# Kernel tuning notes

Measured on AMD Instinct MI355X. Metric: run time of the kernel, lower is better.

Reference implementation:

```python
import jax, jax.numpy as jnp
import numpy as np

B, T, I, H, C = 4096, 64, 60, 60, 600


def setup_inputs() -> dict:
    key = jax.random.key(0)
    ks = jax.random.split(key, 7)
    s = 1.0 / np.sqrt(H).astype(np.float32)  # PyTorch RNN init bound
    u = lambda k, shape: jax.random.uniform(k, shape, jnp.float32, -s, s)
    return {
        "x": jax.random.normal(ks[0], (B, T, I), jnp.float32),
        "w_ih": u(ks[1], (2, 3 * H, I)),   # per-direction [3H, I], gates (r,z,n)
        "w_hh": u(ks[2], (2, 3 * H, H)),
        "b_ih": u(ks[3], (2, 3 * H)),
        "b_hh": u(ks[4], (2, 3 * H)),
        "fc_w": u(ks[5], (C, 2 * H * T)),
        "fc_b": u(ks[6], (C,)),
    }


def _gru_dir(x_tbi, w_ih, w_hh, b_ih, b_hh):
    # Precompute input-side gate pre-activations for all timesteps: [T, B, 3H]
    gx = jnp.einsum('tbi,gi->tbg', x_tbi, w_ih) + b_ih
    h0 = jnp.zeros((x_tbi.shape[1], H), x_tbi.dtype)

    def step(h, gx_t):
        gh = h @ w_hh.T + b_hh                      # [B, 3H]
        r = jax.nn.sigmoid(gx_t[:, :H] + gh[:, :H])
        z = jax.nn.sigmoid(gx_t[:, H:2 * H] + gh[:, H:2 * H])
        n = jnp.tanh(gx_t[:, 2 * H:] + r * gh[:, 2 * H:])
        h_new = (1.0 - z) * n + z * h
        return h_new, h_new

    _, hs = jax.lax.scan(step, h0, gx)
    return hs  # [T, B, H]


def reference(x, w_ih, w_hh, b_ih, b_hh, fc_w, fc_b):
    xt = jnp.swapaxes(x, 0, 1)                        # [T, B, I]
    fwd = _gru_dir(xt, w_ih[0], w_hh[0], b_ih[0], b_hh[0])           # [T,B,H]
    bwd = _gru_dir(xt[::-1], w_ih[1], w_hh[1], b_ih[1], b_hh[1])[::-1]
    out = jnp.concatenate([fwd, bwd], axis=-1)        # [T, B, 2H]
    out = jnp.swapaxes(out, 0, 1).reshape(x.shape[0], -1)  # [B, T*2H]
    return out @ fc_w.T + fc_b
```

## Files before the change

kernel.cpp:

```cpp
#include <hip/hip_runtime.h>

#define BB 4096
#define TT 64
#define NH 60
#define KF 7680
#define NC 600

typedef short bf16x8 __attribute__((ext_vector_type(8)));
typedef float f32x4 __attribute__((ext_vector_type(4)));
#define MFMA16(A,B,C) __builtin_amdgcn_mfma_f32_16x16x32_bf16(A,B,C,0,0,0)

__device__ __forceinline__ unsigned short f2bf(float v) {
    unsigned int u = __float_as_uint(v);
    return (unsigned short)((u + 0x7FFFu + ((u >> 16) & 1u)) >> 16);
}
__device__ __forceinline__ float bf2f(unsigned short b) {
    return __uint_as_float(((unsigned int)b) << 16);
}
__device__ __forceinline__ float sigf(float v)     { return 1.f / (1.f + __expf(-v)); }
__device__ __forceinline__ float tanhfast(float v) { return 2.f / (1.f + __expf(-2.f * v)) - 1.f; }

__global__ __launch_bounds__(512, 2) void gru4_kernel(
    const float* __restrict__ x,
    const float* __restrict__ w_ih,
    const float* __restrict__ w_hh,
    const float* __restrict__ b_ih,
    const float* __restrict__ b_hh,
    unsigned int* __restrict__ hs)
{
    __shared__ unsigned short XHh[2][32 * 128];
    __shared__ unsigned short XHl[2][32 * 128];
    __shared__ unsigned int hstage[2][32][60];

    const int tid = threadIdx.x;
    const int d  = blockIdx.y;
    const int b0 = blockIdx.x * 32;
    const int wave = tid >> 6, lane = tid & 63;
    const int mtile = wave >> 2, ug = wave & 3;
    const int l15 = lane & 15, lq = lane >> 4;
    const int j = ug * 16 + l15;
    const bool jv = j < NH;
    const int m = mtile * 16 + l15;
    const int rbase = mtile * 16 + lq * 4;

    for (int i = tid; i < 2 * 32 * 128; i += 512) { (&XHh[0][0])[i] = 0; (&XHl[0][0])[i] = 0; }

    bf16x8 wHf[3][4], wLf[3][4];
#pragma unroll
    for (int g = 0; g < 3; ++g) {
#pragma unroll
        for (int kt = 0; kt < 4; ++kt) {
            bf16x8 h8, l8;
            const int kb = kt * 32 + lq * 8;
#pragma unroll
            for (int e = 0; e < 8; ++e) {
                const int k = kb + e;
                float v = 0.f;
                if (jv) {
                    if (k < 60)                    v = w_ih[(size_t)d * 10800 + (g * 60 + j) * 60 + k];
                    else if (k >= 64 && k < 124)   v = w_hh[(size_t)d * 10800 + (g * 60 + j) * 60 + (k - 64)];
                }
                const unsigned short hb = f2bf(v);
                const unsigned short lb = f2bf(v - bf2f(hb));
                h8[e] = (short)hb; l8[e] = (short)lb;
            }
            wHf[g][kt] = h8; wLf[g][kt] = l8;
        }
    }

    float bir = 0, biz = 0, bin = 0, bhr = 0, bhz = 0, bhn = 0;
    if (jv) {
        bir = b_ih[d * 180 + j]; biz = b_ih[d * 180 + 60 + j]; bin = b_ih[d * 180 + 120 + j];
        bhr = b_hh[d * 180 + j]; bhz = b_hh[d * 180 + 60 + j]; bhn = b_hh[d * 180 + 120 + j];
    }

    const bool xact = tid < 480;
    const int rowx = xact ? tid / 15 : 31;
    const int cx   = xact ? tid % 15 : 14;
    const float* xb = x + ((size_t)(b0 + rowx) * TT) * 60 + cx * 4;
    unsigned int* hsb = hs + (size_t)(b0 + rowx) * KF + d * 60 + cx * 4;

    __syncthreads();

    if (xact) {
        const int tt0 = d ? (TT - 1) : 0;
        const float4 v = *(const float4*)(xb + tt0 * 60);
        const float vv[4] = {v.x, v.y, v.z, v.w};
#pragma unroll
        for (int e = 0; e < 4; ++e) {
            const int k = cx * 4 + e;
            const int idx = rowx * 128 + (((k >> 3) ^ (rowx & 7)) << 3) + (k & 7);
            const unsigned short hb = f2bf(vv[e]);
            XHh[0][idx] = hb; XHl[0][idx] = f2bf(vv[e] - bf2f(hb));
        }
    }
    float hold[4] = {0.f, 0.f, 0.f, 0.f};
    __syncthreads();

#pragma unroll 2
    for (int s = 0; s < TT; ++s) {
        const int p = s & 1, pn = p ^ 1;
        const int tt = d ? (TT - 1 - s) : s;

        float4 xp = make_float4(0.f, 0.f, 0.f, 0.f);
        const bool morex = (s < TT - 1) && xact;
        if (morex) xp = *(const float4*)(xb + (d ? (TT - 2 - s) : (s + 1)) * 60);

        f32x4 aR0 = {0,0,0,0}, aR1 = {0,0,0,0}, aZ0 = {0,0,0,0}, aZ1 = {0,0,0,0},
              aNX = {0,0,0,0}, aNH_ = {0,0,0,0};
        const unsigned short* Xh = &XHh[p][0];
        const unsigned short* Xl = &XHl[p][0];
#pragma unroll
        for (int kt = 0; kt < 4; ++kt) {
            const int c = kt * 4 + lq;
            const int off = m * 128 + ((c ^ (m & 7)) << 3);
            const bf16x8 aH = *(const bf16x8*)(Xh + off);
            const bf16x8 aL = *(const bf16x8*)(Xl + off);
            if (kt < 2) {
                aR0 = MFMA16(aH, wHf[0][kt], aR0); aR0 = MFMA16(aH, wLf[0][kt], aR0); aR0 = MFMA16(aL, wHf[0][kt], aR0);
                aZ0 = MFMA16(aH, wHf[1][kt], aZ0); aZ0 = MFMA16(aH, wLf[1][kt], aZ0); aZ0 = MFMA16(aL, wHf[1][kt], aZ0);
                aNX = MFMA16(aH, wHf[2][kt], aNX); aNX = MFMA16(aH, wLf[2][kt], aNX); aNX = MFMA16(aL, wHf[2][kt], aNX);
            } else {
                aR1 = MFMA16(aH, wHf[0][kt], aR1); aR1 = MFMA16(aH, wLf[0][kt], aR1); aR1 = MFMA16(aL, wHf[0][kt], aR1);
                aZ1 = MFMA16(aH, wHf[1][kt], aZ1); aZ1 = MFMA16(aH, wLf[1][kt], aZ1); aZ1 = MFMA16(aL, wHf[1][kt], aZ1);
                aNH_ = MFMA16(aH, wHf[2][kt], aNH_); aNH_ = MFMA16(aH, wLf[2][kt], aNH_); aNH_ = MFMA16(aL, wHf[2][kt], aNH_);
            }
        }

        float hnew[4];
#pragma unroll
        for (int r = 0; r < 4; ++r) {
            const float rr = sigf(aR0[r] + aR1[r] + bir + bhr);
            const float zz = sigf(aZ0[r] + aZ1[r] + biz + bhz);
            const float nn = tanhfast(aNX[r] + bin + rr * (aNH_[r] + bhn));
            hnew[r] = (1.f - zz) * nn + zz * hold[r];
            hold[r] = hnew[r];
        }

        if (jv) {
#pragma unroll
            for (int r = 0; r < 4; ++r) {
                const int rw = rbase + r;
                const int k = 64 + j;
                const int idx = rw * 128 + (((k >> 3) ^ (rw & 7)) << 3) + (k & 7);
                const unsigned short hb = f2bf(hnew[r]);
                const unsigned short lb = f2bf(hnew[r] - bf2f(hb));
                XHh[pn][idx] = hb; XHl[pn][idx] = lb;
                hstage[pn][rw][j] = ((unsigned int)hb << 16) | lb;
            }
        }
        if (morex) {
            const float vv[4] = {xp.x, xp.y, xp.z, xp.w};
#pragma unroll
            for (int e = 0; e < 4; ++e) {
                const int k = cx * 4 + e;
                const int idx = rowx * 128 + (((k >> 3) ^ (rowx & 7)) << 3) + (k & 7);
                const unsigned short hb = f2bf(vv[e]);
                XHh[pn][idx] = hb; XHl[pn][idx] = f2bf(vv[e] - bf2f(hb));
            }
        }
        __syncthreads();

        if (xact) {
            const uint4 hv = *(const uint4*)&hstage[pn][rowx][cx * 4];
            *(uint4*)(hsb + (size_t)tt * 120) = hv;
        }
    }
}

__global__ void out_init_kernel(const float* __restrict__ fcb, float* __restrict__ out) {
    const int i = blockIdx.x * 1024 + threadIdx.x;
    out[i] = fcb[i % NC];
}

__global__ __launch_bounds__(512, 2) void fc4_kernel(
    const unsigned int* __restrict__ hs,
    const float* __restrict__ fcw,
    float* __restrict__ out)
{
    __shared__ unsigned short Ash[2][256 * 64];
    __shared__ unsigned short Bsh[2][128 * 64];

    const int tid = threadIdx.x;
    const int m0 = blockIdx.x * 256;
    const int n0 = blockIdx.y * 128;
    const int k0 = blockIdx.z * 2560;
    const int wave = tid >> 6, lane = tid & 63;
    const int wm = wave >> 1, wn = wave & 1;
    const int l15 = lane & 15, lq = lane >> 4;

    f32x4 acc[4][4];
#pragma unroll
    for (int a = 0; a < 4; ++a)
#pragma unroll
        for (int b = 0; b < 4; ++b) acc[a][b] = (f32x4){0, 0, 0, 0};

    uint4 pa[4]; float4 pb[2];

#define STAGE_LOAD(t) do {                                                          \
    const int kc_ = k0 + (t) * 32;                                                  \
    _Pragma("unroll")                                                               \
    for (int it = 0; it < 4; ++it) {                                                \
        const int g_ = tid + it * 512, row_ = g_ >> 3, qi_ = g_ & 7;                \
        pa[it] = *(const uint4*)(hs + (size_t)(m0 + row_) * KF + kc_ + qi_ * 4);    \
    }                                                                               \
    _Pragma("unroll")                                                               \
    for (int it = 0; it < 2; ++it) {                                                \
        const int g_ = tid + it * 512, row_ = g_ >> 3, qi_ = g_ & 7;                \
        const int cc_ = n0 + row_;                                                  \
        pb[it] = (cc_ < NC) ? *(const float4*)(fcw + (size_t)cc_ * KF + kc_ + qi_ * 4) \
                            : make_float4(0.f, 0.f, 0.f, 0.f);                      \
    }                                                                               \
} while (0)

#define STAGE_WRITE(buf) do {                                                       \
    _Pragma("unroll")                                                               \
    for (int it = 0; it < 4; ++it) {                                                \
        const int g_ = tid + it * 512, row_ = g_ >> 3, qi_ = g_ & 7;                \
        const int ch_ = qi_ >> 1, hf_ = qi_ & 1;                                    \
        unsigned short* base_ = &Ash[buf][row_ * 64];                               \
        uint2 wh_, wl_;                                                             \
        wh_.x = (pa[it].x >> 16) | (pa[it].y & 0xFFFF0000u);                        \
        wh_.y = (pa[it].z >> 16) | (pa[it].w & 0xFFFF0000u);                        \
        wl_.x = (pa[it].x & 0xFFFFu) | (pa[it].y << 16);                            \
        wl_.y = (pa[it].z & 0xFFFFu) | (pa[it].w << 16);                            \
        *(uint2*)(base_ + ((ch_ ^ (row_ & 7)) << 3) + hf_ * 4) = wh_;               \
        *(uint2*)(base_ + (((ch_ | 4) ^ (row_ & 7)) << 3) + hf_ * 4) = wl_;         \
    }                                                                               \
    _Pragma("unroll")                                                               \
    for (int it = 0; it < 2; ++it) {                                                \
        const int g_ = tid + it * 512, row_ = g_ >> 3, qi_ = g_ & 7;                \
        const int ch_ = qi_ >> 1, hf_ = qi_ & 1;                                    \
        unsigned short* base_ = &Bsh[buf][row_ * 64];                               \
        const float bv_[4] = {pb[it].x, pb[it].y, pb[it].z, pb[it].w};              \
        unsigned short h4_[4], l4_[4];                                              \
        _Pragma("unroll")                                                           \
        for (int e = 0; e < 4; ++e) { h4_[e] = f2bf(bv_[e]); l4_[e] = f2bf(bv_[e] - bf2f(h4_[e])); } \
        uint2 wh_, wl_;                                                             \
        wh_.x = (unsigned int)h4_[0] | ((unsigned int)h4_[1] << 16);                \
        wh_.y = (unsigned int)h4_[2] | ((unsigned int)h4_[3] << 16);                \
        wl_.x = (unsigned int)l4_[0] | ((unsigned int)l4_[1] << 16);                \
        wl_.y = (unsigned int)l4_[2] | ((unsigned int)l4_[3] << 16);                \
        *(uint2*)(base_ + ((ch_ ^ (row_ & 7)) << 3) + hf_ * 4) = wh_;               \
        *(uint2*)(base_ + (((ch_ | 4) ^ (row_ & 7)) << 3) + hf_ * 4) = wl_;         \
    }                                                                               \
} while (0)

#define MFMA_PHASE(buf) do {                                                        \
    const unsigned short* Ab_ = &Ash[buf][0];                                       \
    const unsigned short* Bb_ = &Bsh[buf][0];                                       \
    bf16x8 aH_[4], aL_[4], bH_[4], bL_[4];                                          \
    _Pragma("unroll")                                                               \
    for (int t = 0; t < 4; ++t) {                                                   \
        const int mr_ = wm * 64 + t * 16 + l15;                                     \
        const unsigned short* p_ = Ab_ + mr_ * 64;                                  \
        aH_[t] = *(const bf16x8*)(p_ + ((lq ^ (mr_ & 7)) << 3));                    \
        aL_[t] = *(const bf16x8*)(p_ + (((lq | 4) ^ (mr_ & 7)) << 3));              \
        const int nr_ = wn * 64 + t * 16 + l15;                                     \
        const unsigned short* q_ = Bb_ + nr_ * 64;                                  \
        bH_[t] = *(const bf16x8*)(q_ + ((lq ^ (nr_ & 7)) << 3));                    \
        bL_[t] = *(const bf16x8*)(q_ + (((lq | 4) ^ (nr_ & 7)) << 3));              \
    }                                                                               \
    _Pragma("unroll")                                                               \
    for (int mt = 0; mt < 4; ++mt)                                                  \
        _Pragma("unroll")                                                           \
        for (int nt = 0; nt < 4; ++nt) {                                            \
            acc[mt][nt] = MFMA16(aH_[mt], bH_[nt], acc[mt][nt]);                    \
            acc[mt][nt] = MFMA16(aH_[mt], bL_[nt], acc[mt][nt]);                    \
            acc[mt][nt] = MFMA16(aL_[mt], bH_[nt], acc[mt][nt]);                    \
        }                                                                           \
} while (0)

#define BARRIER_LGKM() do {                                                         \
    asm volatile("s_waitcnt lgkmcnt(0)" ::: "memory");                              \
    __builtin_amdgcn_s_barrier();                                                   \
    __builtin_amdgcn_sched_barrier(0);                                              \
} while (0)

    STAGE_LOAD(0);
    STAGE_WRITE(0);
    STAGE_LOAD(1);
    __syncthreads();

#pragma unroll 1
    for (int t = 0; t < 80; t += 2) {
        STAGE_WRITE(1);
        if (t + 2 < 80) STAGE_LOAD(t + 2);
        MFMA_PHASE(0);
        BARRIER_LGKM();
        if (t + 2 < 80) STAGE_WRITE(0);
        if (t + 3 < 80) STAGE_LOAD(t + 3);
        MFMA_PHASE(1);
        BARRIER_LGKM();
    }

#pragma unroll
    for (int mt = 0; mt < 4; ++mt) {
        const int row = m0 + wm * 64 + mt * 16 + lq * 4;
#pragma unroll
        for (int nt = 0; nt < 4; ++nt) {
            const int col = n0 + wn * 64 + nt * 16 + l15;
            if (col < NC) {
#pragma unroll
                for (int r = 0; r < 4; ++r)
                    atomicAdd(out + (size_t)(row + r) * NC + col, acc[mt][nt][r]);
            }
        }
    }
#undef STAGE_LOAD
#undef STAGE_WRITE
#undef MFMA_PHASE
#undef BARRIER_LGKM
}

extern "C" void kernel_launch(void* const* d_in, const int* in_sizes, int n_in,
                              void* d_out, int out_size, void* d_ws, size_t ws_size,
                              hipStream_t stream) {
    (void)in_sizes; (void)n_in; (void)out_size;
    const float* x    = (const float*)d_in[0];
    const float* w_ih = (const float*)d_in[1];
    const float* w_hh = (const float*)d_in[2];
    const float* b_ih = (const float*)d_in[3];
    const float* b_hh = (const float*)d_in[4];
    const float* fcw  = (const float*)d_in[5];
    const float* fcb  = (const float*)d_in[6];
    float* out = (float*)d_out;
    unsigned int* hs = (unsigned int*)d_ws;

    if (ws_size < (size_t)KF * BB * sizeof(unsigned int)) return;

    out_init_kernel<<<dim3((BB * NC) / 1024), 1024, 0, stream>>>(fcb, out);
    gru4_kernel<<<dim3(BB / 32, 2), 512, 0, stream>>>(x, w_ih, w_hh, b_ih, b_hh, hs);
    fc4_kernel<<<dim3(BB / 256, 5, 3), 512, 0, stream>>>(hs, fcw, out);
}
```

Baseline: 365.6 us.

## Shrink GRU blocks, use direct global-to-LDS loads and drop FC weight low part

```diff
diff --git a/kernel.cpp b/kernel.cpp
--- a/kernel.cpp
+++ b/kernel.cpp
@@ -10,6 +10,9 @@
 typedef float f32x4 __attribute__((ext_vector_type(4)));
 #define MFMA16(A,B,C) __builtin_amdgcn_mfma_f32_16x16x32_bf16(A,B,C,0,0,0)
 
+typedef const __attribute__((address_space(1))) unsigned int* gas_u32;
+typedef __attribute__((address_space(3))) unsigned int* las_u32;
+
 __device__ __forceinline__ unsigned short f2bf(float v) {
     unsigned int u = __float_as_uint(v);
     return (unsigned short)((u + 0x7FFFu + ((u >> 16) & 1u)) >> 16);
@@ -20,7 +23,21 @@
 __device__ __forceinline__ float sigf(float v)     { return 1.f / (1.f + __expf(-v)); }
 __device__ __forceinline__ float tanhfast(float v) { return 2.f / (1.f + __expf(-2.f * v)) - 1.f; }
 
-__global__ __launch_bounds__(512, 2) void gru4_kernel(
+__device__ __forceinline__ void unpk(const uint4 a, const uint4 b, bf16x8& hi, bf16x8& lo) {
+    uint4 h, l;
+    h.x = (a.x >> 16) | (a.y & 0xFFFF0000u);
+    h.y = (a.z >> 16) | (a.w & 0xFFFF0000u);
+    h.z = (b.x >> 16) | (b.y & 0xFFFF0000u);
+    h.w = (b.z >> 16) | (b.w & 0xFFFF0000u);
+    l.x = (a.x & 0xFFFFu) | (a.y << 16);
+    l.y = (a.z & 0xFFFFu) | (a.w << 16);
+    l.z = (b.x & 0xFFFFu) | (b.y << 16);
+    l.w = (b.z & 0xFFFFu) | (b.w << 16);
+    hi = __builtin_bit_cast(bf16x8, h);
+    lo = __builtin_bit_cast(bf16x8, l);
+}
+
+__global__ __launch_bounds__(256, 2) void gru5_kernel(
     const float* __restrict__ x,
     const float* __restrict__ w_ih,
     const float* __restrict__ w_hh,
@@ -28,22 +45,22 @@
     const float* __restrict__ b_hh,
     unsigned int* __restrict__ hs)
 {
-    __shared__ unsigned short XHh[2][32 * 128];
-    __shared__ unsigned short XHl[2][32 * 128];
-    __shared__ unsigned int hstage[2][32][60];
+    __shared__ unsigned short XHh[2][16 * 128];
+    __shared__ unsigned short XHl[2][16 * 128];
+    __shared__ unsigned int hstage[2][16][60];
 
     const int tid = threadIdx.x;
     const int d  = blockIdx.y;
-    const int b0 = blockIdx.x * 32;
+    const int b0 = blockIdx.x * 16;
     const int wave = tid >> 6, lane = tid & 63;
-    const int mtile = wave >> 2, ug = wave & 3;
+    const int ug = wave;
     const int l15 = lane & 15, lq = lane >> 4;
     const int j = ug * 16 + l15;
     const bool jv = j < NH;
-    const int m = mtile * 16 + l15;
-    const int rbase = mtile * 16 + lq * 4;
-
-    for (int i = tid; i < 2 * 32 * 128; i += 512) { (&XHh[0][0])[i] = 0; (&XHl[0][0])[i] = 0; }
+    const int m = l15;
+    const int rbase = lq * 4;
+
+    for (int i = tid; i < 2 * 16 * 128; i += 256) { (&XHh[0][0])[i] = 0; (&XHl[0][0])[i] = 0; }
 
     bf16x8 wHf[3][4], wLf[3][4];
 #pragma unroll
@@ -74,8 +91,8 @@
         bhr = b_hh[d * 180 + j]; bhz = b_hh[d * 180 + 60 + j]; bhn = b_hh[d * 180 + 120 + j];
     }
 
-    const bool xact = tid < 480;
-    const int rowx = xact ? tid / 15 : 31;
+    const bool xact = tid < 240;
+    const int rowx = xact ? tid / 15 : 15;
     const int cx   = xact ? tid % 15 : 14;
     const float* xb = x + ((size_t)(b0 + rowx) * TT) * 60 + cx * 4;
     unsigned int* hsb = hs + (size_t)(b0 + rowx) * KF + d * 60 + cx * 4;
@@ -97,7 +114,7 @@
     float hold[4] = {0.f, 0.f, 0.f, 0.f};
     __syncthreads();
 
-#pragma unroll 2
+#pragma unroll 1
     for (int s = 0; s < TT; ++s) {
         const int p = s & 1, pn = p ^ 1;
         const int tt = d ? (TT - 1 - s) : s;
@@ -173,18 +190,18 @@
     out[i] = fcb[i % NC];
 }
 
-__global__ __launch_bounds__(512, 2) void fc4_kernel(
+__global__ __launch_bounds__(512, 1) void fc5_kernel(
     const unsigned int* __restrict__ hs,
     const float* __restrict__ fcw,
     float* __restrict__ out)
 {
-    __shared__ unsigned short Ash[2][256 * 64];
-    __shared__ unsigned short Bsh[2][128 * 64];
+    __shared__ unsigned int  Apk[2][256 * 32];
+    __shared__ unsigned short Bs[2][128 * 32];
 
     const int tid = threadIdx.x;
     const int m0 = blockIdx.x * 256;
     const int n0 = blockIdx.y * 128;
-    const int k0 = blockIdx.z * 2560;
+    const int k0 = blockIdx.z * 1280;
     const int wave = tid >> 6, lane = tid & 63;
     const int wm = wave >> 1, wn = wave & 1;
     const int l15 = lane & 15, lq = lane >> 4;
@@ -195,103 +212,94 @@
 #pragma unroll
         for (int b = 0; b < 4; ++b) acc[a][b] = (f32x4){0, 0, 0, 0};
 
-    uint4 pa[4]; float4 pb[2];
-
-#define STAGE_LOAD(t) do {                                                          \
-    const int kc_ = k0 + (t) * 32;                                                  \
-    _Pragma("unroll")                                                               \
-    for (int it = 0; it < 4; ++it) {                                                \
-        const int g_ = tid + it * 512, row_ = g_ >> 3, qi_ = g_ & 7;                \
-        pa[it] = *(const uint4*)(hs + (size_t)(m0 + row_) * KF + kc_ + qi_ * 4);    \
-    }                                                                               \
-    _Pragma("unroll")                                                               \
-    for (int it = 0; it < 2; ++it) {                                                \
-        const int g_ = tid + it * 512, row_ = g_ >> 3, qi_ = g_ & 7;                \
-        const int cc_ = n0 + row_;                                                  \
-        pb[it] = (cc_ < NC) ? *(const float4*)(fcw + (size_t)cc_ * KF + kc_ + qi_ * 4) \
-                            : make_float4(0.f, 0.f, 0.f, 0.f);                      \
-    }                                                                               \
+    const int ga_row = lane >> 3;
+    const int ga_chk = (lane & 7) ^ ga_row;
+
+#define STAGE_A(buf, kc_) do {                                                        \
+    _Pragma("unroll")                                                                 \
+    for (int c_ = 0; c_ < 4; ++c_) {                                                  \
+        const int bc_ = wave * 4 + c_;                                                \
+        const unsigned int* g_ = hs + (size_t)(m0 + bc_ * 8 + ga_row) * KF            \
+                                    + (kc_) + (ga_chk << 2);                          \
+        __builtin_amdgcn_global_load_lds((gas_u32)g_, (las_u32)&Apk[buf][bc_ * 256],  \
+                                         16, 0, 0);                                   \
+    }                                                                                 \
 } while (0)
 
-#define STAGE_WRITE(buf) do {                                                       \
-    _Pragma("unroll")                                                               \
-    for (int it = 0; it < 4; ++it) {                                                \
-        const int g_ = tid + it * 512, row_ = g_ >> 3, qi_ = g_ & 7;                \
-        const int ch_ = qi_ >> 1, hf_ = qi_ & 1;                                    \
-        unsigned short* base_ = &Ash[buf][row_ * 64];                               \
-        uint2 wh_, wl_;                                                             \
-        wh_.x = (pa[it].x >> 16) | (pa[it].y & 0xFFFF0000u);                        \
-        wh_.y = (pa[it].z >> 16) | (pa[it].w & 0xFFFF0000u);                        \
-        wl_.x = (pa[it].x & 0xFFFFu) | (pa[it].y << 16);                            \
-        wl_.y = (pa[it].z & 0xFFFFu) | (pa[it].w << 16);                            \
-        *(uint2*)(base_ + ((ch_ ^ (row_ & 7)) << 3) + hf_ * 4) = wh_;               \
-        *(uint2*)(base_ + (((ch_ | 4) ^ (row_ & 7)) << 3) + hf_ * 4) = wl_;         \
-    }                                                                               \
-    _Pragma("unroll")                                                               \
-    for (int it = 0; it < 2; ++it) {                                                \
-        const int g_ = tid + it * 512, row_ = g_ >> 3, qi_ = g_ & 7;                \
-        const int ch_ = qi_ >> 1, hf_ = qi_ & 1;                                    \
-        unsigned short* base_ = &Bsh[buf][row_ * 64];                               \
-        const float bv_[4] = {pb[it].x, pb[it].y, pb[it].z, pb[it].w};              \
-        unsigned short h4_[4], l4_[4];                                              \
-        _Pragma("unroll")                                                           \
-        for (int e = 0; e < 4; ++e) { h4_[e] = f2bf(bv_[e]); l4_[e] = f2bf(bv_[e] - bf2f(h4_[e])); } \
-        uint2 wh_, wl_;                                                             \
-        wh_.x = (unsigned int)h4_[0] | ((unsigned int)h4_[1] << 16);                \
-        wh_.y = (unsigned int)h4_[2] | ((unsigned int)h4_[3] << 16);                \
-        wl_.x = (unsigned int)l4_[0] | ((unsigned int)l4_[1] << 16);                \
-        wl_.y = (unsigned int)l4_[2] | ((unsigned int)l4_[3] << 16);                \
-        *(uint2*)(base_ + ((ch_ ^ (row_ & 7)) << 3) + hf_ * 4) = wh_;               \
-        *(uint2*)(base_ + (((ch_ | 4) ^ (row_ & 7)) << 3) + hf_ * 4) = wl_;         \
-    }                                                                               \
+    float4 pb[2];
+#define LOAD_B(kc_) do {                                                              \
+    _Pragma("unroll")                                                                 \
+    for (int it = 0; it < 2; ++it) {                                                  \
+        const int g_ = tid + it * 512, row_ = g_ >> 3, qi_ = g_ & 7;                  \
+        const int cc_ = n0 + row_;                                                    \
+        pb[it] = (cc_ < NC) ? *(const float4*)(fcw + (size_t)cc_ * KF + (kc_) + qi_ * 4) \
+                            : make_float4(0.f, 0.f, 0.f, 0.f);                        \
+    }                                                                                 \
 } while (0)
 
-#define MFMA_PHASE(buf) do {                                                        \
-    const unsigned short* Ab_ = &Ash[buf][0];                                       \
-    const unsigned short* Bb_ = &Bsh[buf][0];                                       \
-    bf16x8 aH_[4], aL_[4], bH_[4], bL_[4];                                          \
-    _Pragma("unroll")                                                               \
-    for (int t = 0; t < 4; ++t) {                                                   \
-        const int mr_ = wm * 64 + t * 16 + l15;                                     \
-        const unsigned short* p_ = Ab_ + mr_ * 64;                                  \
-        aH_[t] = *(const bf16x8*)(p_ + ((lq ^ (mr_ & 7)) << 3));                    \
-        aL_[t] = *(const bf16x8*)(p_ + (((lq | 4) ^ (mr_ & 7)) << 3));              \
-        const int nr_ = wn * 64 + t * 16 + l15;                                     \
-        const unsigned short* q_ = Bb_ + nr_ * 64;                                  \
-        bH_[t] = *(const bf16x8*)(q_ + ((lq ^ (nr_ & 7)) << 3));                    \
-        bL_[t] = *(const bf16x8*)(q_ + (((lq | 4) ^ (nr_ & 7)) << 3));              \
-    }                                                                               \
-    _Pragma("unroll")                                                               \
-    for (int mt = 0; mt < 4; ++mt)                                                  \
-        _Pragma("unroll")                                                           \
-        for (int nt = 0; nt < 4; ++nt) {                                            \
-            acc[mt][nt] = MFMA16(aH_[mt], bH_[nt], acc[mt][nt]);                    \
-            acc[mt][nt] = MFMA16(aH_[mt], bL_[nt], acc[mt][nt]);                    \
-            acc[mt][nt] = MFMA16(aL_[mt], bH_[nt], acc[mt][nt]);                    \
-        }                                                                           \
+#define WRITE_B(buf) do {                                                             \
+    _Pragma("unroll")                                                                 \
+    for (int it = 0; it < 2; ++it) {                                                  \
+        const int g_ = tid + it * 512, row_ = g_ >> 3, qi_ = g_ & 7;                  \
+        const int ch_ = qi_ >> 1, hf_ = qi_ & 1;                                      \
+        unsigned short* base_ = &Bs[buf][row_ * 32];                                  \
+        const float bv_[4] = {pb[it].x, pb[it].y, pb[it].z, pb[it].w};                \
+        unsigned short h4_[4];                                                        \
+        _Pragma("unroll")                                                             \
+        for (int e = 0; e < 4; ++e) h4_[e] = f2bf(bv_[e]);                            \
+        uint2 wv_;                                                                    \
+        wv_.x = (unsigned int)h4_[0] | ((unsigned int)h4_[1] << 16);                  \
+        wv_.y = (unsigned int)h4_[2] | ((unsigned int)h4_[3] << 16);                  \
+        *(uint2*)(base_ + ((ch_ ^ (row_ & 3)) << 3) + hf_ * 4) = wv_;                 \
+    }                                                                                 \
 } while (0)
 
-#define BARRIER_LGKM() do {                                                         \
-    asm volatile("s_waitcnt lgkmcnt(0)" ::: "memory");                              \
-    __builtin_amdgcn_s_barrier();                                                   \
-    __builtin_amdgcn_sched_barrier(0);                                              \
+#define MFMA_PHASE(buf) do {                                                          \
+    bf16x8 aH_[4], aL_[4], bH_[4];                                                    \
+    _Pragma("unroll")                                                                 \
+    for (int t = 0; t < 4; ++t) {                                                     \
+        const int mr_ = wm * 64 + t * 16 + l15;                                       \
+        const unsigned int* pr_ = &Apk[buf][mr_ * 32];                                \
+        const int q0_ = (2 * lq) ^ (mr_ & 7);                                         \
+        const int q1_ = (2 * lq + 1) ^ (mr_ & 7);                                     \
+        const uint4 c0_ = *(const uint4*)(pr_ + q0_ * 4);                             \
+        const uint4 c1_ = *(const uint4*)(pr_ + q1_ * 4);                             \
+        unpk(c0_, c1_, aH_[t], aL_[t]);                                               \
+        const int nr_ = wn * 64 + t * 16 + l15;                                       \
+        bH_[t] = *(const bf16x8*)(&Bs[buf][nr_ * 32] + ((lq ^ (nr_ & 3)) << 3));      \
+    }                                                                                 \
+    _Pragma("unroll")                                                                 \
+    for (int mt = 0; mt < 4; ++mt)                                                    \
+        _Pragma("unroll")                                                             \
+        for (int nt = 0; nt < 4; ++nt) {                                              \
+            acc[mt][nt] = MFMA16(aH_[mt], bH_[nt], acc[mt][nt]);                      \
+            acc[mt][nt] = MFMA16(aL_[mt], bH_[nt], acc[mt][nt]);                      \
+        }                                                                             \
 } while (0)
 
-    STAGE_LOAD(0);
-    STAGE_WRITE(0);
-    STAGE_LOAD(1);
-    __syncthreads();
+    STAGE_A(0, k0);
+    LOAD_B(k0);
+    asm volatile("s_waitcnt vmcnt(0)" ::: "memory");
+    WRITE_B(0);
+    asm volatile("s_waitcnt lgkmcnt(0)" ::: "memory");
+    __builtin_amdgcn_s_barrier();
+    __builtin_amdgcn_sched_barrier(0);
 
 #pragma unroll 1
-    for (int t = 0; t < 80; t += 2) {
-        STAGE_WRITE(1);
-        if (t + 2 < 80) STAGE_LOAD(t + 2);
-        MFMA_PHASE(0);
-        BARRIER_LGKM();
-        if (t + 2 < 80) STAGE_WRITE(0);
-        if (t + 3 < 80) STAGE_LOAD(t + 3);
-        MFMA_PHASE(1);
-        BARRIER_LGKM();
+    for (int t = 0; t < 40; ++t) {
+        const int cur = t & 1, nxt = cur ^ 1;
+        const bool more = (t + 1) < 40;
+        if (more) {
+            STAGE_A(nxt, k0 + (t + 1) * 32);
+            LOAD_B(k0 + (t + 1) * 32);
+        }
+        MFMA_PHASE(cur);
+        asm volatile("s_waitcnt vmcnt(0)" ::: "memory");
+        __builtin_amdgcn_sched_barrier(0);
+        if (more) WRITE_B(nxt);
+        asm volatile("s_waitcnt lgkmcnt(0)" ::: "memory");
+        __builtin_amdgcn_s_barrier();
+        __builtin_amdgcn_sched_barrier(0);
     }
 
 #pragma unroll
@@ -307,10 +315,10 @@
             }
         }
     }
-#undef STAGE_LOAD
-#undef STAGE_WRITE
+#undef STAGE_A
+#undef LOAD_B
+#undef WRITE_B
 #undef MFMA_PHASE
-#undef BARRIER_LGKM
 }
 
 extern "C" void kernel_launch(void* const* d_in, const int* in_sizes, int n_in,
@@ -330,6 +338,6 @@
     if (ws_size < (size_t)KF * BB * sizeof(unsigned int)) return;
 
     out_init_kernel<<<dim3((BB * NC) / 1024), 1024, 0, stream>>>(fcb, out);
-    gru4_kernel<<<dim3(BB / 32, 2), 512, 0, stream>>>(x, w_ih, w_hh, b_ih, b_hh, hs);
-    fc4_kernel<<<dim3(BB / 256, 5, 3), 512, 0, stream>>>(hs, fcw, out);
-}
+    gru5_kernel<<<dim3(BB / 16, 2), 256, 0, stream>>>(x, w_ih, w_hh, b_ih, b_hh, hs);
+    fc5_kernel<<<dim3(BB / 256, 5, 6), 512, 0, stream>>>(hs, fcw, out);
+}
```

Result: slower. 419.4 us (+14.7%).
